# Kernel optimization log

Hardware: AMD Instinct MI355X
Metric: run time of the kernel (lower is better)

Reference implementation:

```python
import jax, jax.numpy as jnp
import numpy as np

N = 100_000   # nodes
E = 1_600_000 # edges (avg degree 16)
D = 128       # input_dim
H = 128       # hidden_dim
G = 64        # graphs in batch
C = 2         # num_classes


def setup_inputs() -> dict:
    key = jax.random.key(0)
    ks = jax.random.split(key, 16)
    x = jax.random.normal(ks[0], (N, D), dtype=jnp.float32)
    edge_index = jax.random.randint(ks[1], (2, E), 0, N, dtype=jnp.int32)
    batch = jnp.sort(jax.random.randint(ks[2], (N,), 0, G, dtype=jnp.int32))
    def lin(k, fin, fout):
        s = 1.0 / np.sqrt(fin)
        kw, kb = jax.random.split(k)
        W = jax.random.uniform(kw, (fin, fout), jnp.float32, -s, s)
        b = jax.random.uniform(kb, (fout,), jnp.float32, -s, s)
        return W, b
    W0, b0 = lin(ks[3], D, H)
    W1, b1 = lin(ks[4], H, H)
    W2, b2 = lin(ks[5], H, H)
    Wc1, bc1 = lin(ks[6], 2 * H, H)
    Wc2, bc2 = lin(ks[7], H, C)
    return dict(x=x, edge_index=edge_index, batch=batch,
                W0=W0, b0=b0, W1=W1, b1=b1, W2=W2, b2=b2,
                Wc1=Wc1, bc1=bc1, Wc2=Wc2, bc2=bc2)


def _gcn_layer(x, W, b, src, dst, dinv):
    # GCNConv with self-loops and symmetric normalization:
    # out_i = sum_{j->i} d_j^{-1/2} d_i^{-1/2} (x_j W) + d_i^{-1} (x_i W) + b
    h = x @ W                                   # [N, H]
    coef = dinv[src] * dinv[dst]                # [E]
    agg = jax.ops.segment_sum(h[src] * coef[:, None], dst, num_segments=N)
    return agg + h * (dinv * dinv)[:, None] + b


def reference(x, edge_index, batch, W0, b0, W1, b1, W2, b2, Wc1, bc1, Wc2, bc2):
    src, dst = edge_index[0], edge_index[1]
    # degree with self-loops (in-degree on target nodes + 1)
    deg = jax.ops.segment_sum(jnp.ones((E,), jnp.float32), dst, num_segments=N) + 1.0
    dinv = jax.lax.rsqrt(deg)
    for W, b in ((W0, b0), (W1, b1), (W2, b2)):
        x = jax.nn.relu(_gcn_layer(x, W, b, src, dst, dinv))
        # dropout: inference mode -> identity
    # global mean pool per graph
    sums = jax.ops.segment_sum(x, batch, num_segments=G)            # [G, H]
    cnt = jax.ops.segment_sum(jnp.ones((N,), jnp.float32), batch, num_segments=G)
    pooled = sums / jnp.maximum(cnt, 1.0)[:, None]
    combined = jnp.concatenate([pooled, pooled], axis=1)            # [G, 2H]
    hcls = jax.nn.relu(combined @ Wc1 + bc1)
    return hcls @ Wc2 + bc2                                         # [G, C]
```

## Files before the change

kernel.cpp:

```cpp
#include <hip/hip_runtime.h>

#define HDIM 128
#define GCOUNT 64
#define CHUNK 2048

__device__ __forceinline__ float bfl(unsigned u) { return __uint_as_float(u << 16); }
__device__ __forceinline__ unsigned short f2bf(float f) {
  unsigned u = __float_as_uint(f);
  unsigned r = (u + 0x7fffu + ((u >> 16) & 1u)) >> 16;
  return (unsigned short)r;
}
__device__ __forceinline__ unsigned pk2(float a, float b) {
  return (unsigned)f2bf(a) | ((unsigned)f2bf(b) << 16);
}

typedef __attribute__((ext_vector_type(8))) short short8;
typedef __attribute__((ext_vector_type(4))) float f32x4;

__device__ __forceinline__ unsigned qb(float v, float rinv) {
  int q = (int)rintf(v * rinv);
  return (unsigned)(q & 0xff);
}


__global__ void mega1(const float* __restrict__ W0, const float* __restrict__ W1,
                      const float* __restrict__ W2,
                      unsigned short* __restrict__ h0, unsigned short* __restrict__ l0,
                      unsigned short* __restrict__ h1, unsigned short* __restrict__ l1,
                      unsigned short* __restrict__ h2, unsigned short* __restrict__ l2,
                      float* __restrict__ pooled, float* __restrict__ gcnt, int pz,
                      const int* __restrict__ dst, int E, int G, int NB1,
                      int* __restrict__ gcount,
                      const float* __restrict__ x, uint2* __restrict__ S,
                      uint2* __restrict__ Sb, float* __restrict__ csaP,
                      float* __restrict__ csbP,
                      float* __restrict__ cs_base, int n) {
  __shared__ int hist[512];
  int b = blockIdx.x, t = threadIdx.x;
  if (b < 192) {
    int w = b >> 6;
    int idx = (b & 63) * 256 + t;
    const float* W = (w == 0) ? W0 : (w == 1) ? W1 : W2;
    unsigned short* hi = (w == 0) ? h0 : (w == 1) ? h1 : h2;
    unsigned short* lo = (w == 0) ? l0 : (w == 1) ? l1 : l2;
    int k = idx >> 7, nn = idx & 127;
    float wv = W[idx];
    unsigned short h = f2bf(wv);
    float hf = __uint_as_float((unsigned)h << 16);
    unsigned short l = f2bf(wv - hf);
    int kb = k >> 5, quad = (k >> 3) & 3, e = k & 7;
    int nt = nn >> 4, m = nn & 15;
    int di = (((kb * 8 + nt) * 64) + quad * 16 + m) * 8 + e;
    hi[di] = h;
    lo[di] = l;
  } else if (b < 192 + pz) {
    int i = (b - 192) * 256 + t;
    if (i < GCOUNT * HDIM) pooled[i] = 0.f;
    else if (i - GCOUNT * HDIM < GCOUNT) gcnt[i - GCOUNT * HDIM] = 0.f;
    if (b == 192) {
      if (t < 16) S[(size_t)n * 16 + t] = make_uint2(0u, 0u);
      else if (t < 32) Sb[(size_t)n * 16 + (t - 16)] = make_uint2(0u, 0u);
      else if (t == 32) csaP[n] = 0.f;
      else if (t == 33) csbP[n] = 0.f;
    }
  } else if (b < 192 + pz + G) {
    int blk = b - 192 - pz;
    for (int i = t; i < NB1; i += 256) hist[i] = 0;
    __syncthreads();
    int base = blk * CHUNK;
    #pragma unroll
    for (int j = 0; j < CHUNK / 256; j++) {
      int e = base + j * 256 + t;
      if (e < E) atomicAdd(&hist[dst[e] >> 8], 1);
    }
    __syncthreads();
    for (int i = t; i < NB1; i += 256) gcount[i * G + blk] = hist[i];
  } else {
    int idx = (b - 192 - pz - G) * 16 + (t >> 4);
    int l = t & 15;
    int ridx = min(idx, n - 1);
    float4 f0 = ((const float4*)x)[(size_t)ridx * 32 + l * 2];
    float4 f1 = ((const float4*)x)[(size_t)ridx * 32 + l * 2 + 1];
    float v0 = f0.x, v1 = f0.y, v2 = f0.z, v3 = f0.w;
    float v4 = f1.x, v5 = f1.y, v6 = f1.z, v7 = f1.w;
    float mx = fmaxf(fmaxf(fmaxf(fabsf(v0), fabsf(v1)), fmaxf(fabsf(v2), fabsf(v3))),
                     fmaxf(fmaxf(fabsf(v4), fabsf(v5)), fmaxf(fabsf(v6), fabsf(v7))));
    mx = fmaxf(mx, __shfl_xor(mx, 1));
    mx = fmaxf(mx, __shfl_xor(mx, 2));
    mx = fmaxf(mx, __shfl_xor(mx, 4));
    mx = fmaxf(mx, __shfl_xor(mx, 8));
    float c = mx * (1.0f / 127.0f);
    float rinv = (mx > 0.f) ? 127.0f / mx : 0.f;
    if (idx < n) {
      unsigned lo = qb(v0, rinv) | (qb(v1, rinv) << 8) | (qb(v2, rinv) << 16) | (qb(v3, rinv) << 24);
      unsigned hi = qb(v4, rinv) | (qb(v5, rinv) << 8) | (qb(v6, rinv) << 16) | (qb(v7, rinv) << 24);
      S[(size_t)idx * 16 + l] = make_uint2(lo, hi);
      if (l == 0) cs_base[idx] = c;
    }
  }
}


__global__ void scanA(int* __restrict__ g, int* __restrict__ bsum, int M) {
  __shared__ int sh[1024];
  int t = threadIdx.x;
  int i = blockIdx.x * 1024 + t;
  int v = (i < M) ? g[i] : 0;
  sh[t] = v;
  __syncthreads();
  for (int off = 1; off < 1024; off <<= 1) {
    int u = (t >= off) ? sh[t - off] : 0;
    __syncthreads();
    sh[t] += u;
    __syncthreads();
  }
  if (i < M) g[i] = sh[t] - v;
  if (t == 1023) bsum[blockIdx.x] = sh[1023];
}


__global__ void rs_scatter(const int* __restrict__ src, const int* __restrict__ dst,
                           const int* __restrict__ gscan, const int* __restrict__ bsum,
                           int nb, int E, int G, int NB1,
                           unsigned* __restrict__ sp) {
  __shared__ int run[512];
  __shared__ int sb[512];
  int blk = blockIdx.x, t = threadIdx.x;
  sb[t] = (t < nb) ? bsum[t] : 0;
  __syncthreads();
  for (int off = 1; off < 512; off <<= 1) {
    int u = (t >= off) ? sb[t - off] : 0;
    __syncthreads();
    sb[t] += u;
    __syncthreads();
  }
  for (int i = t; i < NB1; i += 512) {
    int idx = i * G + blk;
    int j = idx >> 10;
    run[i] = gscan[idx] + (j ? sb[j - 1] : 0);
  }
  __syncthreads();
  int base = blk * CHUNK;
  #pragma unroll
  for (int j = 0; j < CHUNK / 512; j++) {
    int e = base + j * 512 + t;
    if (e < E) {
      int d = dst[e];
      int pos = atomicAdd(&run[d >> 8], 1);
      sp[pos] = (unsigned)src[e] | ((unsigned)(d & 255) << 24);
    }
  }
}


__global__ void csr_fine(const unsigned* __restrict__ sp, const int* __restrict__ gscan,
                         const int* __restrict__ bsum, int nb,
                         int E, int G, int NB1,
                         int2* __restrict__ rowpe, int* __restrict__ colv,
                         float* __restrict__ dinv, const float* __restrict__ cs_base,
                         float* __restrict__ cs, int n) {
  __shared__ int sb[512];
  __shared__ int hist[256];
  __shared__ int scn[256];
  __shared__ int run2[256];
  int hb = blockIdx.x, t = threadIdx.x;
  sb[t] = (t < nb) ? bsum[t] : 0;
  __syncthreads();
  for (int off = 1; off < 512; off <<= 1) {
    int u = (t >= off) ? sb[t - off] : 0;
    __syncthreads();
    sb[t] += u;
    __syncthreads();
  }
  int iO = hb * G;
  int jO = iO >> 10;
  int O = gscan[iO] + (jO ? sb[jO - 1] : 0);
  int Oe;
  if (hb == NB1 - 1) Oe = E;
  else {
    int i2 = (hb + 1) * G;
    int j2 = i2 >> 10;
    Oe = gscan[i2] + (j2 ? sb[j2 - 1] : 0);
  }
  int PO = ((O + 3) & ~3) + hb * 1024;
  if (t < 256) hist[t] = 0;
  __syncthreads();
  for (int e = O + t; e < Oe; e += 512) atomicAdd(&hist[sp[e] >> 24], 1);
  __syncthreads();
  int v = 0, pv = 0;
  if (t < 256) { v = hist[t]; pv = (v + 3) & ~3; scn[t] = pv; }
  __syncthreads();
  for (int off = 1; off < 256; off <<= 1) {
    int u = (t < 256 && t >= off) ? scn[t - off] : 0;
    __syncthreads();
    if (t < 256) scn[t] += u;
    __syncthreads();
  }
  if (t < 256) {
    int st = PO + scn[t] - pv;
    run2[t] = st;
    int d = (hb << 8) + t;
    rowpe[d] = make_int2(st, st + pv);
    for (int i = v; i < pv; i++) colv[st + i] = n;
    if (d < n) {
      float dv = rsqrtf((float)v + 1.0f);
      dinv[d] = dv;
      cs[d] = cs_base[d] * dv;
    }
  }
  __syncthreads();
  for (int e = O + t; e < Oe; e += 512) {
    unsigned p = sp[e];
    int pos = atomicAdd(&run2[p >> 24], 1);
    colv[pos] = (int)(p & 0xFFFFFFu);
  }
}


__device__ __forceinline__ void acc8(uint2 v, float c, float* a) {
  int xx = (int)v.x, yy = (int)v.y;
  a[0] += c * (float)(signed char)(xx);
  a[1] += c * (float)(signed char)(xx >> 8);
  a[2] += c * (float)(signed char)(xx >> 16);
  a[3] += c * (float)(xx >> 24);
  a[4] += c * (float)(signed char)(yy);
  a[5] += c * (float)(signed char)(yy >> 8);
  a[6] += c * (float)(signed char)(yy >> 16);
  a[7] += c * (float)(yy >> 24);
}


__device__ __forceinline__ void agg_phase(
    const uint2* __restrict__ S, const float* __restrict__ cs,
    const float* __restrict__ dinv,
    const int2* __restrict__ rowpe,
    const int* __restrict__ col,
    uint4* At, int block0, int t, int n) {
  int grp = t >> 4, gl = t & 15;
  #pragma unroll 1
  for (int k = 0; k < 4; k++) {
    int lrow = grp * 4 + k;
    int g = block0 + lrow;
    uint4 o = make_uint4(0u, 0u, 0u, 0u);
    if (g < n) {
      float a[8];
      {
        uint2 q = S[(size_t)g * 16 + gl];
        float c = cs[g];
        int xx = (int)q.x, yy = (int)q.y;
        a[0] = c * (float)(signed char)(xx);
        a[1] = c * (float)(signed char)(xx >> 8);
        a[2] = c * (float)(signed char)(xx >> 16);
        a[3] = c * (float)(xx >> 24);
        a[4] = c * (float)(signed char)(yy);
        a[5] = c * (float)(signed char)(yy >> 8);
        a[6] = c * (float)(signed char)(yy >> 16);
        a[7] = c * (float)(yy >> 24);
      }
      int2 pe = rowpe[g];
      int e = pe.x, e1 = pe.y;
      if (e < e1) {
        int4 ca = *(const int4*)(col + e);
        uint2 q0 = S[(size_t)ca.x * 16 + gl];
        uint2 q1 = S[(size_t)ca.y * 16 + gl];
        uint2 q2 = S[(size_t)ca.z * 16 + gl];
        uint2 q3 = S[(size_t)ca.w * 16 + gl];
        float c0 = cs[ca.x], c1 = cs[ca.y], c2 = cs[ca.z], c3 = cs[ca.w];
        #pragma unroll 1
        for (e += 4; e < e1; e += 4) {
          int4 cn = *(const int4*)(col + e);
          uint2 p0 = S[(size_t)cn.x * 16 + gl];
          uint2 p1 = S[(size_t)cn.y * 16 + gl];
          uint2 p2 = S[(size_t)cn.z * 16 + gl];
          uint2 p3 = S[(size_t)cn.w * 16 + gl];
          float d0 = cs[cn.x], d1 = cs[cn.y], d2 = cs[cn.z], d3 = cs[cn.w];
          acc8(q0, c0, a); acc8(q1, c1, a); acc8(q2, c2, a); acc8(q3, c3, a);
          q0 = p0; q1 = p1; q2 = p2; q3 = p3;
          c0 = d0; c1 = d1; c2 = d2; c3 = d3;
        }
        acc8(q0, c0, a); acc8(q1, c1, a); acc8(q2, c2, a); acc8(q3, c3, a);
      }
      float d = dinv[g];
      o.x = pk2(a[0] * d, a[1] * d);
      o.y = pk2(a[2] * d, a[3] * d);
      o.z = pk2(a[4] * d, a[5] * d);
      o.w = pk2(a[6] * d, a[7] * d);
    }
    At[(gl << 6) + (lrow ^ (gl & 7))] = o;
  }
}

__device__ __forceinline__ void stage16(uint4* Wl, const uint4* __restrict__ WT, int t) {
  #pragma unroll
  for (int i = 0; i < 4; i++) {
    int idx = t + i * 256;
    Wl[idx] = WT[idx];
  }
}

__device__ __forceinline__ void mfma2(const uint4* Wl, const uint4* av, f32x4* acc,
                                      int kbase, int lane) {
  #pragma unroll
  for (int kk = 0; kk < 2; kk++) {
    short8 af = __builtin_bit_cast(short8, av[kbase + kk]);
    #pragma unroll
    for (int nt = 0; nt < 8; nt++) {
      uint4 b = Wl[(kk * 8 + nt) * 64 + lane];
      acc[nt] = __builtin_amdgcn_mfma_f32_16x16x32_bf16(af, __builtin_bit_cast(short8, b), acc[nt], 0, 0, 0);
    }
  }
}

__global__ __launch_bounds__(256, 4) void fused_q8(
    const uint2* __restrict__ S, const float* __restrict__ cs,
    const float* __restrict__ dinv,
    const int2* __restrict__ rowpe,
    const int* __restrict__ col,
    const uint4* __restrict__ WThi, const uint4* __restrict__ WTlo,
    const float* __restrict__ bias,
    unsigned char* __restrict__ Sout, float* __restrict__ csout, int n) {
  __shared__ __align__(16) char smem[16384];
  uint4* At = (uint4*)smem;
  uint4* Wl = (uint4*)smem;
  int t = threadIdx.x;
  int lane = t & 63, wv = t >> 6;
  int m = lane & 15, quad = lane >> 4;
  int block0 = blockIdx.x * 64;

  agg_phase(S, cs, dinv, rowpe, col, At, block0, t, n);
  __syncthreads();

  uint4 av[4];
  #pragma unroll
  for (int kb = 0; kb < 4; kb++) {
    int glr = kb * 4 + quad;
    av[kb] = At[(glr << 6) + ((wv * 16 + m) ^ (glr & 7))];
  }
  __syncthreads();

  f32x4 acc[8];
  #pragma unroll
  for (int i = 0; i < 8; i++) acc[i] = (f32x4){0.f, 0.f, 0.f, 0.f};

  stage16(Wl, WThi, t);        __syncthreads();
  mfma2(Wl, av, acc, 0, lane); __syncthreads();
  stage16(Wl, WThi + 1024, t); __syncthreads();
  mfma2(Wl, av, acc, 2, lane); __syncthreads();
  stage16(Wl, WTlo, t);        __syncthreads();
  mfma2(Wl, av, acc, 0, lane); __syncthreads();
  stage16(Wl, WTlo + 1024, t); __syncthreads();
  mfma2(Wl, av, acc, 2, lane); __syncthreads();

  char* stg = smem;
  float* LcA = (float*)(smem + 9216);
  #pragma unroll
  for (int r = 0; r < 4; r++) {
    int lrow = wv * 16 + quad * 4 + r;
    int grow = block0 + lrow;
    float sc = (grow < n) ? dinv[grow] : 0.f;
    float v[8];
    float mx = 0.f;
    #pragma unroll
    for (int nt = 0; nt < 8; nt++) {
      v[nt] = fmaxf(acc[nt][r] + bias[nt * 16 + m], 0.f) * sc;
      mx = fmaxf(mx, v[nt]);
    }
    mx = fmaxf(mx, __shfl_xor(mx, 1));
    mx = fmaxf(mx, __shfl_xor(mx, 2));
    mx = fmaxf(mx, __shfl_xor(mx, 4));
    mx = fmaxf(mx, __shfl_xor(mx, 8));
    float c = mx * (1.0f / 127.0f);
    float rinv = (mx > 0.f) ? 127.0f / mx : 0.f;
    #pragma unroll
    for (int nt = 0; nt < 8; nt++) {
      stg[lrow * 144 + nt * 16 + m] = (char)(int)rintf(v[nt] * rinv);
    }
    if (m == 0) LcA[lrow] = c;
  }
  __syncthreads();
  for (int i = t; i < 512; i += 256) {
    int lrow = i >> 3, seg = i & 7;
    int grow = block0 + lrow;
    if (grow < n)
      ((uint4*)Sout)[(size_t)grow * 8 + seg] = *(const uint4*)&stg[lrow * 144 + seg * 16];
  }
  if (t < 64 && block0 + t < n) csout[block0 + t] = LcA[t];
}

__global__ __launch_bounds__(256, 4) void fused_final(
    const uint2* __restrict__ S, const float* __restrict__ cs,
    const float* __restrict__ dinv,
    const int2* __restrict__ rowpe,
    const int* __restrict__ col,
    const uint4* __restrict__ WThi, const uint4* __restrict__ WTlo,
    const float* __restrict__ bias, const int* __restrict__ batch,
    float* __restrict__ pooled, float* __restrict__ gcnt, int n) {
  __shared__ __align__(16) char smem[16384];
  uint4* At = (uint4*)smem;
  uint4* Wl = (uint4*)smem;
  int t = threadIdx.x;
  int lane = t & 63, wv = t >> 6;
  int m = lane & 15, quad = lane >> 4;
  int block0 = blockIdx.x * 64;

  agg_phase(S, cs, dinv, rowpe, col, At, block0, t, n);
  __syncthreads();

  uint4 av[4];
  #pragma unroll
  for (int kb = 0; kb < 4; kb++) {
    int glr = kb * 4 + quad;
    av[kb] = At[(glr << 6) + ((wv * 16 + m) ^ (glr & 7))];
  }
  __syncthreads();

  f32x4 acc[8];
  #pragma unroll
  for (int i = 0; i < 8; i++) acc[i] = (f32x4){0.f, 0.f, 0.f, 0.f};

  stage16(Wl, WThi, t);        __syncthreads();
  mfma2(Wl, av, acc, 0, lane); __syncthreads();
  stage16(Wl, WThi + 1024, t); __syncthreads();
  mfma2(Wl, av, acc, 2, lane); __syncthreads();
  stage16(Wl, WTlo, t);        __syncthreads();
  mfma2(Wl, av, acc, 0, lane); __syncthreads();
  stage16(Wl, WTlo + 1024, t); __syncthreads();
  mfma2(Wl, av, acc, 2, lane); __syncthreads();

  unsigned short* Ls = (unsigned short*)smem;
  #pragma unroll
  for (int r = 0; r < 4; r++) {
    int lrow = wv * 16 + quad * 4 + r;
    #pragma unroll
    for (int nt = 0; nt < 8; nt++) {
      float v = fmaxf(acc[nt][r] + bias[nt * 16 + m], 0.f);
      Ls[lrow * 128 + nt * 16 + m] = f2bf(v);
    }
  }
  __syncthreads();
  if (t < 128) {
    float a2 = 0.f, cl = 0.f;
    int gcur = -1;
    for (int r = 0; r < 64; r++) {
      int grow = block0 + r;
      if (grow >= n) break;
      int gr = batch[grow];
      if (gr != gcur) {
        if (gcur >= 0) {
          atomicAdd(&pooled[gcur * HDIM + t], a2);
          if (t == 0) atomicAdd(&gcnt[gcur], cl);
        }
        a2 = 0.f; cl = 0.f; gcur = gr;
      }
      a2 += bfl((unsigned)Ls[r * 128 + t]);
      cl += 1.f;
    }
    if (gcur >= 0) {
      atomicAdd(&pooled[gcur * HDIM + t], a2);
      if (t == 0) atomicAdd(&gcnt[gcur], cl);
    }
  }
}


__global__ void cls_kernel(const float* __restrict__ pooled, const float* __restrict__ gcnt,
                           const float* __restrict__ Wc1, const float* __restrict__ bc1,
                           const float* __restrict__ Wc2, const float* __restrict__ bc2,
                           float* __restrict__ out) {
  __shared__ float p[HDIM];
  __shared__ float r0s[HDIM], r1s[HDIM];
  int g = blockIdx.x, t = threadIdx.x;
  float c = fmaxf(gcnt[g], 1.0f);
  p[t] = pooled[g * HDIM + t] / c;
  __syncthreads();
  float acc = bc1[t];
  for (int k = 0; k < HDIM; k++) {
    acc += p[k] * (Wc1[k * HDIM + t] + Wc1[(HDIM + k) * HDIM + t]);
  }
  float h = fmaxf(acc, 0.f);
  r0s[t] = h * Wc2[t * 2 + 0];
  r1s[t] = h * Wc2[t * 2 + 1];
  __syncthreads();
  for (int s2 = 64; s2 > 0; s2 >>= 1) {
    if (t < s2) { r0s[t] += r0s[t + s2]; r1s[t] += r1s[t + s2]; }
    __syncthreads();
  }
  if (t == 0) {
    out[g * 2 + 0] = r0s[0] + bc2[0];
    out[g * 2 + 1] = r1s[0] + bc2[1];
  }
}


extern "C" void kernel_launch(void* const* d_in, const int* in_sizes, int n_in,
                              void* d_out, int out_size, void* d_ws, size_t ws_size,
                              hipStream_t stream) {
  const float* x   = (const float*)d_in[0];
  const int*   ei  = (const int*)d_in[1];
  const int*   bat = (const int*)d_in[2];
  const float* W0  = (const float*)d_in[3];
  const float* b0  = (const float*)d_in[4];
  const float* W1  = (const float*)d_in[5];
  const float* b1  = (const float*)d_in[6];
  const float* W2  = (const float*)d_in[7];
  const float* b2  = (const float*)d_in[8];
  const float* Wc1 = (const float*)d_in[9];
  const float* bc1 = (const float*)d_in[10];
  const float* Wc2 = (const float*)d_in[11];
  const float* bc2 = (const float*)d_in[12];
  float* out = (float*)d_out;

  int N = in_sizes[0] / HDIM;
  int E = in_sizes[1] / 2;
  const int* src = ei;
  const int* dst = ei + E;

  int NB1 = (N + 255) >> 8;
  int G = (E + CHUNK - 1) / CHUNK;
  int M = NB1 * G;

  char* ws = (char*)d_ws;
  size_t off = 0;
  auto alloc = [&](size_t bytes) -> void* {
    void* p = (void*)(ws + off);
    off += (bytes + 511) & ~(size_t)511;
    return p;
  };
  unsigned char* Sa = (unsigned char*)alloc((size_t)(N + 1) * HDIM * 2);
  unsigned char* Sb = Sa + (size_t)(N + 1) * HDIM;
  float* csa  = (float*)alloc((size_t)(N + 2) * 4);
  float* csb  = (float*)alloc((size_t)(N + 2) * 4);
  float* cs_base = (float*)alloc((size_t)N * 4);
  float* dinv = (float*)alloc((size_t)N * 4);
  int2*  rowpe = (int2*)alloc((size_t)(NB1 * 256 + 2) * 8);
  int*   colv = (int*)alloc((size_t)(E + NB1 * 1024 + 1024) * 4);
  unsigned* sp = (unsigned*)alloc((size_t)E * 4);
  float* pooled = (float*)alloc((size_t)GCOUNT * HDIM * 4);
  float* gcnt   = (float*)alloc((size_t)GCOUNT * 4);
  unsigned short* wt_hi[3], *wt_lo[3];
  for (int i = 0; i < 3; i++) {
    wt_hi[i] = (unsigned short*)alloc(HDIM * HDIM * 2);
    wt_lo[i] = (unsigned short*)alloc(HDIM * HDIM * 2);
  }
  int* gcount = (int*)alloc((size_t)(M + 2) * 4);
  int nbM = (M + 1023) / 1024;
  int* bsum = (int*)alloc((size_t)nbM * 4);

  int pz = (GCOUNT * HDIM + GCOUNT + 255) / 256;
  int psb = (N + 15) / 16;
  mega1<<<192 + pz + G + psb, 256, 0, stream>>>(W0, W1, W2,
      wt_hi[0], wt_lo[0], wt_hi[1], wt_lo[1], wt_hi[2], wt_lo[2],
      pooled, gcnt, pz, dst, E, G, NB1, gcount,
      x, (uint2*)Sa, (uint2*)Sb, csa, csb, cs_base, N);

  scanA<<<nbM, 1024, 0, stream>>>(gcount, bsum, M);

  rs_scatter<<<G, 512, 0, stream>>>(src, dst, gcount, bsum, nbM, E, G, NB1, sp);
  csr_fine<<<NB1, 512, 0, stream>>>(sp, gcount, bsum, nbM, E, G, NB1, rowpe, colv,
      dinv, cs_base, csa, N);

  int fusedBlocks = (N + 63) / 64;

  fused_q8<<<fusedBlocks, 256, 0, stream>>>((const uint2*)Sa, csa, dinv, rowpe, colv,
      (const uint4*)wt_hi[0], (const uint4*)wt_lo[0], b0, Sb, csb, N);

  fused_q8<<<fusedBlocks, 256, 0, stream>>>((const uint2*)Sb, csb, dinv, rowpe, colv,
      (const uint4*)wt_hi[1], (const uint4*)wt_lo[1], b1, Sa, csa, N);

  fused_final<<<fusedBlocks, 256, 0, stream>>>((const uint2*)Sa, csa, dinv, rowpe, colv,
      (const uint4*)wt_hi[2], (const uint4*)wt_lo[2], b2, bat, pooled, gcnt, N);

  cls_kernel<<<GCOUNT, HDIM, 0, stream>>>(pooled, gcnt, Wc1, bc1, Wc2, bc2, out);
}
```

Measured before the change: 318.1 us.

## Halve rows per block in fused GCN kernels and split output columns across waves

Each fused layer block now handles 32 nodes instead of 64, giving twice as many blocks. The four waves are arranged as two row halves by two column halves, each computing 4 of the 8 MFMA output tiles. The per-row int8 quantisation max is now combined across the two column-half waves through shared memory, which adds a barrier. This is meant to improve latency hiding and load balance in the gather-bound aggregation, at the cost of restaging the weight matrix twice as often per node.

Measured after the change: 322.7 us. Within noise of the previous version (+1.4%).

```diff
diff --git a/kernel.cpp b/kernel.cpp
--- a/kernel.cpp
+++ b/kernel.cpp
@@ -238,8 +238,8 @@
     uint4* At, int block0, int t, int n) {
   int grp = t >> 4, gl = t & 15;
   #pragma unroll 1
-  for (int k = 0; k < 4; k++) {
-    int lrow = grp * 4 + k;
+  for (int k = 0; k < 2; k++) {
+    int lrow = grp * 2 + k;
     int g = block0 + lrow;
     uint4 o = make_uint4(0u, 0u, 0u, 0u);
     if (g < n) {
@@ -286,7 +286,7 @@
       o.z = pk2(a[4] * d, a[5] * d);
       o.w = pk2(a[6] * d, a[7] * d);
     }
-    At[(gl << 6) + (lrow ^ (gl & 7))] = o;
+    At[(gl << 5) + (lrow ^ (gl & 7))] = o;
   }
 }
 
@@ -298,15 +298,15 @@
   }
 }
 
-__device__ __forceinline__ void mfma2(const uint4* Wl, const uint4* av, f32x4* acc,
-                                      int kbase, int lane) {
+__device__ __forceinline__ void mfma2h(const uint4* Wl, const uint4* av, f32x4* acc,
+                                       int kbase, int nh, int lane) {
   #pragma unroll
   for (int kk = 0; kk < 2; kk++) {
     short8 af = __builtin_bit_cast(short8, av[kbase + kk]);
     #pragma unroll
-    for (int nt = 0; nt < 8; nt++) {
-      uint4 b = Wl[(kk * 8 + nt) * 64 + lane];
-      acc[nt] = __builtin_amdgcn_mfma_f32_16x16x32_bf16(af, __builtin_bit_cast(short8, b), acc[nt], 0, 0, 0);
+    for (int j = 0; j < 4; j++) {
+      uint4 b = Wl[(kk * 8 + nh + j) * 64 + lane];
+      acc[j] = __builtin_amdgcn_mfma_f32_16x16x32_bf16(af, __builtin_bit_cast(short8, b), acc[j], 0, 0, 0);
     }
   }
 }
@@ -325,7 +325,10 @@
   int t = threadIdx.x;
   int lane = t & 63, wv = t >> 6;
   int m = lane & 15, quad = lane >> 4;
-  int block0 = blockIdx.x * 64;
+  int rh = wv >> 1;
+  int nh = (wv & 1) * 4;
+  int r0 = rh * 16;
+  int block0 = blockIdx.x * 32;
 
   agg_phase(S, cs, dinv, rowpe, col, At, block0, t, n);
   __syncthreads();
@@ -334,57 +337,66 @@
   #pragma unroll
   for (int kb = 0; kb < 4; kb++) {
     int glr = kb * 4 + quad;
-    av[kb] = At[(glr << 6) + ((wv * 16 + m) ^ (glr & 7))];
-  }
-  __syncthreads();
-
-  f32x4 acc[8];
-  #pragma unroll
-  for (int i = 0; i < 8; i++) acc[i] = (f32x4){0.f, 0.f, 0.f, 0.f};
-
-  stage16(Wl, WThi, t);        __syncthreads();
-  mfma2(Wl, av, acc, 0, lane); __syncthreads();
-  stage16(Wl, WThi + 1024, t); __syncthreads();
-  mfma2(Wl, av, acc, 2, lane); __syncthreads();
-  stage16(Wl, WTlo, t);        __syncthreads();
-  mfma2(Wl, av, acc, 0, lane); __syncthreads();
-  stage16(Wl, WTlo + 1024, t); __syncthreads();
-  mfma2(Wl, av, acc, 2, lane); __syncthreads();
+    av[kb] = At[(glr << 5) + ((r0 + m) ^ (glr & 7))];
+  }
+  __syncthreads();
+
+  f32x4 acc[4];
+  #pragma unroll
+  for (int i = 0; i < 4; i++) acc[i] = (f32x4){0.f, 0.f, 0.f, 0.f};
+
+  stage16(Wl, WThi, t);              __syncthreads();
+  mfma2h(Wl, av, acc, 0, nh, lane);  __syncthreads();
+  stage16(Wl, WThi + 1024, t);       __syncthreads();
+  mfma2h(Wl, av, acc, 2, nh, lane);  __syncthreads();
+  stage16(Wl, WTlo, t);              __syncthreads();
+  mfma2h(Wl, av, acc, 0, nh, lane);  __syncthreads();
+  stage16(Wl, WTlo + 1024, t);       __syncthreads();
+  mfma2h(Wl, av, acc, 2, nh, lane);  __syncthreads();
 
   char* stg = smem;
-  float* LcA = (float*)(smem + 9216);
+  float* LcA = (float*)(smem + 4608);
+  float* pmx = (float*)(smem + 4864);
+  float v[4][4];
   #pragma unroll
   for (int r = 0; r < 4; r++) {
-    int lrow = wv * 16 + quad * 4 + r;
+    int lrow = r0 + quad * 4 + r;
     int grow = block0 + lrow;
     float sc = (grow < n) ? dinv[grow] : 0.f;
-    float v[8];
     float mx = 0.f;
     #pragma unroll
-    for (int nt = 0; nt < 8; nt++) {
-      v[nt] = fmaxf(acc[nt][r] + bias[nt * 16 + m], 0.f) * sc;
-      mx = fmaxf(mx, v[nt]);
+    for (int j = 0; j < 4; j++) {
+      v[r][j] = fmaxf(acc[j][r] + bias[(nh + j) * 16 + m], 0.f) * sc;
+      mx = fmaxf(mx, v[r][j]);
     }
     mx = fmaxf(mx, __shfl_xor(mx, 1));
     mx = fmaxf(mx, __shfl_xor(mx, 2));
     mx = fmaxf(mx, __shfl_xor(mx, 4));
     mx = fmaxf(mx, __shfl_xor(mx, 8));
-    float c = mx * (1.0f / 127.0f);
-    float rinv = (mx > 0.f) ? 127.0f / mx : 0.f;
+    if (m == 0) pmx[wv * 16 + quad * 4 + r] = mx;
+  }
+  __syncthreads();
+  #pragma unroll
+  for (int r = 0; r < 4; r++) {
+    int lr = quad * 4 + r;
+    int lrow = r0 + lr;
+    float full = fmaxf(pmx[(rh * 2) * 16 + lr], pmx[(rh * 2 + 1) * 16 + lr]);
+    float c = full * (1.0f / 127.0f);
+    float rinv = (full > 0.f) ? 127.0f / full : 0.f;
     #pragma unroll
-    for (int nt = 0; nt < 8; nt++) {
-      stg[lrow * 144 + nt * 16 + m] = (char)(int)rintf(v[nt] * rinv);
-    }
-    if (m == 0) LcA[lrow] = c;
-  }
-  __syncthreads();
-  for (int i = t; i < 512; i += 256) {
-    int lrow = i >> 3, seg = i & 7;
+    for (int j = 0; j < 4; j++) {
+      stg[lrow * 144 + (nh + j) * 16 + m] = (char)(int)rintf(v[r][j] * rinv);
+    }
+    if (m == 0 && nh == 0) LcA[lrow] = c;
+  }
+  __syncthreads();
+  {
+    int lrow = t >> 3, seg = t & 7;
     int grow = block0 + lrow;
     if (grow < n)
       ((uint4*)Sout)[(size_t)grow * 8 + seg] = *(const uint4*)&stg[lrow * 144 + seg * 16];
   }
-  if (t < 64 && block0 + t < n) csout[block0 + t] = LcA[t];
+  if (t < 32 && block0 + t < n) csout[block0 + t] = LcA[t];
 }
 
 __global__ __launch_bounds__(256, 4) void fused_final(
@@ -401,7 +413,10 @@
   int t = threadIdx.x;
   int lane = t & 63, wv = t >> 6;
   int m = lane & 15, quad = lane >> 4;
-  int block0 = blockIdx.x * 64;
+  int rh = wv >> 1;
+  int nh = (wv & 1) * 4;
+  int r0 = rh * 16;
+  int block0 = blockIdx.x * 32;
 
   agg_phase(S, cs, dinv, rowpe, col, At, block0, t, n);
   __syncthreads();
@@ -410,38 +425,38 @@
   #pragma unroll
   for (int kb = 0; kb < 4; kb++) {
     int glr = kb * 4 + quad;
-    av[kb] = At[(glr << 6) + ((wv * 16 + m) ^ (glr & 7))];
-  }
-  __syncthreads();
-
-  f32x4 acc[8];
-  #pragma unroll
-  for (int i = 0; i < 8; i++) acc[i] = (f32x4){0.f, 0.f, 0.f, 0.f};
-
-  stage16(Wl, WThi, t);        __syncthreads();
-  mfma2(Wl, av, acc, 0, lane); __syncthreads();
-  stage16(Wl, WThi + 1024, t); __syncthreads();
-  mfma2(Wl, av, acc, 2, lane); __syncthreads();
-  stage16(Wl, WTlo, t);        __syncthreads();
-  mfma2(Wl, av, acc, 0, lane); __syncthreads();
-  stage16(Wl, WTlo + 1024, t); __syncthreads();
-  mfma2(Wl, av, acc, 2, lane); __syncthreads();
+    av[kb] = At[(glr << 5) + ((r0 + m) ^ (glr & 7))];
+  }
+  __syncthreads();
+
+  f32x4 acc[4];
+  #pragma unroll
+  for (int i = 0; i < 4; i++) acc[i] = (f32x4){0.f, 0.f, 0.f, 0.f};
+
+  stage16(Wl, WThi, t);              __syncthreads();
+  mfma2h(Wl, av, acc, 0, nh, lane);  __syncthreads();
+  stage16(Wl, WThi + 1024, t);       __syncthreads();
+  mfma2h(Wl, av, acc, 2, nh, lane);  __syncthreads();
+  stage16(Wl, WTlo, t);              __syncthreads();
+  mfma2h(Wl, av, acc, 0, nh, lane);  __syncthreads();
+  stage16(Wl, WTlo + 1024, t);       __syncthreads();
+  mfma2h(Wl, av, acc, 2, nh, lane);  __syncthreads();
 
   unsigned short* Ls = (unsigned short*)smem;
   #pragma unroll
   for (int r = 0; r < 4; r++) {
-    int lrow = wv * 16 + quad * 4 + r;
+    int lrow = r0 + quad * 4 + r;
     #pragma unroll
-    for (int nt = 0; nt < 8; nt++) {
-      float v = fmaxf(acc[nt][r] + bias[nt * 16 + m], 0.f);
-      Ls[lrow * 128 + nt * 16 + m] = f2bf(v);
+    for (int j = 0; j < 4; j++) {
+      float v = fmaxf(acc[j][r] + bias[(nh + j) * 16 + m], 0.f);
+      Ls[lrow * 128 + (nh + j) * 16 + m] = f2bf(v);
     }
   }
   __syncthreads();
   if (t < 128) {
     float a2 = 0.f, cl = 0.f;
     int gcur = -1;
-    for (int r = 0; r < 64; r++) {
+    for (int r = 0; r < 32; r++) {
       int grow = block0 + r;
       if (grow >= n) break;
       int gr = batch[grow];
@@ -559,7 +574,7 @@
   csr_fine<<<NB1, 512, 0, stream>>>(sp, gcount, bsum, nbM, E, G, NB1, rowpe, colv,
       dinv, cs_base, csa, N);
 
-  int fusedBlocks = (N + 63) / 64;
+  int fusedBlocks = (N + 31) / 32;
 
   fused_q8<<<fusedBlocks, 256, 0, stream>>>((const uint2*)Sa, csa, dinv, rowpe, colv,
       (const uint4*)wt_hi[0], (const uint4*)wt_lo[0], b0, Sb, csb, N);
```

## Use 1024-thread blocks so each aggregation thread handles one row

Applied to the files above, without the earlier changes.

The fused GCN layer kernels now run 1024 threads per 64-row block instead of 256. Each 16-lane group aggregates a single node row rather than looping over four rows serially, so more gather latency can be hidden. The MFMA work is split across 16 waves, with four row groups each covering two of the eight output column tiles. The per-row int8 quantisation max now needs a cross-wave reduction through shared memory and an extra barrier. The trade-offs are more barrier cost across 16 waves and a tighter launch-bound register budget.

Measured after the change: 354.0 us. 1.11x slower.

```diff
diff --git a/kernel.cpp b/kernel.cpp
--- a/kernel.cpp
+++ b/kernel.cpp
@@ -237,81 +237,74 @@
     const int* __restrict__ col,
     uint4* At, int block0, int t, int n) {
   int grp = t >> 4, gl = t & 15;
-  #pragma unroll 1
-  for (int k = 0; k < 4; k++) {
-    int lrow = grp * 4 + k;
-    int g = block0 + lrow;
-    uint4 o = make_uint4(0u, 0u, 0u, 0u);
-    if (g < n) {
-      float a[8];
-      {
-        uint2 q = S[(size_t)g * 16 + gl];
-        float c = cs[g];
-        int xx = (int)q.x, yy = (int)q.y;
-        a[0] = c * (float)(signed char)(xx);
-        a[1] = c * (float)(signed char)(xx >> 8);
-        a[2] = c * (float)(signed char)(xx >> 16);
-        a[3] = c * (float)(xx >> 24);
-        a[4] = c * (float)(signed char)(yy);
-        a[5] = c * (float)(signed char)(yy >> 8);
-        a[6] = c * (float)(signed char)(yy >> 16);
-        a[7] = c * (float)(yy >> 24);
+  int lrow = grp;
+  int g = block0 + lrow;
+  uint4 o = make_uint4(0u, 0u, 0u, 0u);
+  if (g < n) {
+    float a[8];
+    {
+      uint2 q = S[(size_t)g * 16 + gl];
+      float c = cs[g];
+      int xx = (int)q.x, yy = (int)q.y;
+      a[0] = c * (float)(signed char)(xx);
+      a[1] = c * (float)(signed char)(xx >> 8);
+      a[2] = c * (float)(signed char)(xx >> 16);
+      a[3] = c * (float)(xx >> 24);
+      a[4] = c * (float)(signed char)(yy);
+      a[5] = c * (float)(signed char)(yy >> 8);
+      a[6] = c * (float)(signed char)(yy >> 16);
+      a[7] = c * (float)(yy >> 24);
+    }
+    int2 pe = rowpe[g];
+    int e = pe.x, e1 = pe.y;
+    if (e < e1) {
+      int4 ca = *(const int4*)(col + e);
+      uint2 q0 = S[(size_t)ca.x * 16 + gl];
+      uint2 q1 = S[(size_t)ca.y * 16 + gl];
+      uint2 q2 = S[(size_t)ca.z * 16 + gl];
+      uint2 q3 = S[(size_t)ca.w * 16 + gl];
+      float c0 = cs[ca.x], c1 = cs[ca.y], c2 = cs[ca.z], c3 = cs[ca.w];
+      #pragma unroll 1
+      for (e += 4; e < e1; e += 4) {
+        int4 cn = *(const int4*)(col + e);
+        uint2 p0 = S[(size_t)cn.x * 16 + gl];
+        uint2 p1 = S[(size_t)cn.y * 16 + gl];
+        uint2 p2 = S[(size_t)cn.z * 16 + gl];
+        uint2 p3 = S[(size_t)cn.w * 16 + gl];
+        float d0 = cs[cn.x], d1 = cs[cn.y], d2 = cs[cn.z], d3 = cs[cn.w];
+        acc8(q0, c0, a); acc8(q1, c1, a); acc8(q2, c2, a); acc8(q3, c3, a);
+        q0 = p0; q1 = p1; q2 = p2; q3 = p3;
+        c0 = d0; c1 = d1; c2 = d2; c3 = d3;
       }
-      int2 pe = rowpe[g];
-      int e = pe.x, e1 = pe.y;
-      if (e < e1) {
-        int4 ca = *(const int4*)(col + e);
-        uint2 q0 = S[(size_t)ca.x * 16 + gl];
-        uint2 q1 = S[(size_t)ca.y * 16 + gl];
-        uint2 q2 = S[(size_t)ca.z * 16 + gl];
-        uint2 q3 = S[(size_t)ca.w * 16 + gl];
-        float c0 = cs[ca.x], c1 = cs[ca.y], c2 = cs[ca.z], c3 = cs[ca.w];
-        #pragma unroll 1
-        for (e += 4; e < e1; e += 4) {
-          int4 cn = *(const int4*)(col + e);
-          uint2 p0 = S[(size_t)cn.x * 16 + gl];
-          uint2 p1 = S[(size_t)cn.y * 16 + gl];
-          uint2 p2 = S[(size_t)cn.z * 16 + gl];
-          uint2 p3 = S[(size_t)cn.w * 16 + gl];
-          float d0 = cs[cn.x], d1 = cs[cn.y], d2 = cs[cn.z], d3 = cs[cn.w];
-          acc8(q0, c0, a); acc8(q1, c1, a); acc8(q2, c2, a); acc8(q3, c3, a);
-          q0 = p0; q1 = p1; q2 = p2; q3 = p3;
-          c0 = d0; c1 = d1; c2 = d2; c3 = d3;
-        }
-        acc8(q0, c0, a); acc8(q1, c1, a); acc8(q2, c2, a); acc8(q3, c3, a);
-      }
-      float d = dinv[g];
-      o.x = pk2(a[0] * d, a[1] * d);
-      o.y = pk2(a[2] * d, a[3] * d);
-      o.z = pk2(a[4] * d, a[5] * d);
-      o.w = pk2(a[6] * d, a[7] * d);
-    }
-    At[(gl << 6) + (lrow ^ (gl & 7))] = o;
-  }
+      acc8(q0, c0, a); acc8(q1, c1, a); acc8(q2, c2, a); acc8(q3, c3, a);
+    }
+    float d = dinv[g];
+    o.x = pk2(a[0] * d, a[1] * d);
+    o.y = pk2(a[2] * d, a[3] * d);
+    o.z = pk2(a[4] * d, a[5] * d);
+    o.w = pk2(a[6] * d, a[7] * d);
+  }
+  At[(gl << 6) + (lrow ^ (gl & 7))] = o;
 }
 
 __device__ __forceinline__ void stage16(uint4* Wl, const uint4* __restrict__ WT, int t) {
-  #pragma unroll
-  for (int i = 0; i < 4; i++) {
-    int idx = t + i * 256;
-    Wl[idx] = WT[idx];
-  }
-}
-
-__device__ __forceinline__ void mfma2(const uint4* Wl, const uint4* av, f32x4* acc,
-                                      int kbase, int lane) {
+  Wl[t] = WT[t];
+}
+
+__device__ __forceinline__ void mfma2q(const uint4* Wl, const uint4* av, f32x4* acc,
+                                       int kbase, int nq, int lane) {
   #pragma unroll
   for (int kk = 0; kk < 2; kk++) {
     short8 af = __builtin_bit_cast(short8, av[kbase + kk]);
     #pragma unroll
-    for (int nt = 0; nt < 8; nt++) {
-      uint4 b = Wl[(kk * 8 + nt) * 64 + lane];
-      acc[nt] = __builtin_amdgcn_mfma_f32_16x16x32_bf16(af, __builtin_bit_cast(short8, b), acc[nt], 0, 0, 0);
-    }
-  }
-}
-
-__global__ __launch_bounds__(256, 4) void fused_q8(
+    for (int j = 0; j < 2; j++) {
+      uint4 b = Wl[(kk * 8 + nq + j) * 64 + lane];
+      acc[j] = __builtin_amdgcn_mfma_f32_16x16x32_bf16(af, __builtin_bit_cast(short8, b), acc[j], 0, 0, 0);
+    }
+  }
+}
+
+__global__ __launch_bounds__(1024, 8) void fused_q8(
     const uint2* __restrict__ S, const float* __restrict__ cs,
     const float* __restrict__ dinv,
     const int2* __restrict__ rowpe,
@@ -325,6 +318,9 @@
   int t = threadIdx.x;
   int lane = t & 63, wv = t >> 6;
   int m = lane & 15, quad = lane >> 4;
+  int rg = wv >> 2;
+  int nq = (wv & 3) * 2;
+  int r0 = rg * 16;
   int block0 = blockIdx.x * 64;
 
   agg_phase(S, cs, dinv, rowpe, col, At, block0, t, n);
@@ -334,52 +330,63 @@
   #pragma unroll
   for (int kb = 0; kb < 4; kb++) {
     int glr = kb * 4 + quad;
-    av[kb] = At[(glr << 6) + ((wv * 16 + m) ^ (glr & 7))];
-  }
-  __syncthreads();
-
-  f32x4 acc[8];
-  #pragma unroll
-  for (int i = 0; i < 8; i++) acc[i] = (f32x4){0.f, 0.f, 0.f, 0.f};
-
-  stage16(Wl, WThi, t);        __syncthreads();
-  mfma2(Wl, av, acc, 0, lane); __syncthreads();
-  stage16(Wl, WThi + 1024, t); __syncthreads();
-  mfma2(Wl, av, acc, 2, lane); __syncthreads();
-  stage16(Wl, WTlo, t);        __syncthreads();
-  mfma2(Wl, av, acc, 0, lane); __syncthreads();
-  stage16(Wl, WTlo + 1024, t); __syncthreads();
-  mfma2(Wl, av, acc, 2, lane); __syncthreads();
+    av[kb] = At[(glr << 6) + ((r0 + m) ^ (glr & 7))];
+  }
+  __syncthreads();
+
+  f32x4 acc[2];
+  #pragma unroll
+  for (int i = 0; i < 2; i++) acc[i] = (f32x4){0.f, 0.f, 0.f, 0.f};
+
+  stage16(Wl, WThi, t);               __syncthreads();
+  mfma2q(Wl, av, acc, 0, nq, lane);   __syncthreads();
+  stage16(Wl, WThi + 1024, t);        __syncthreads();
+  mfma2q(Wl, av, acc, 2, nq, lane);   __syncthreads();
+  stage16(Wl, WTlo, t);               __syncthreads();
+  mfma2q(Wl, av, acc, 0, nq, lane);   __syncthreads();
+  stage16(Wl, WTlo + 1024, t);        __syncthreads();
+  mfma2q(Wl, av, acc, 2, nq, lane);   __syncthreads();
 
   char* stg = smem;
   float* LcA = (float*)(smem + 9216);
+  float* pmx = (float*)(smem + 9472);
+  float v[4][2];
   #pragma unroll
   for (int r = 0; r < 4; r++) {
-    int lrow = wv * 16 + quad * 4 + r;
-    int grow = block0 + lrow;
+    int lr = quad * 4 + r;
+    int grow = block0 + r0 + lr;
     float sc = (grow < n) ? dinv[grow] : 0.f;
-    float v[8];
     float mx = 0.f;
     #pragma unroll
-    for (int nt = 0; nt < 8; nt++) {
-      v[nt] = fmaxf(acc[nt][r] + bias[nt * 16 + m], 0.f) * sc;
-      mx = fmaxf(mx, v[nt]);
+    for (int j = 0; j < 2; j++) {
+      v[r][j] = fmaxf(acc[j][r] + bias[(nq + j) * 16 + m], 0.f) * sc;
+      mx = fmaxf(mx, v[r][j]);
     }
     mx = fmaxf(mx, __shfl_xor(mx, 1));
     mx = fmaxf(mx, __shfl_xor(mx, 2));
     mx = fmaxf(mx, __shfl_xor(mx, 4));
     mx = fmaxf(mx, __shfl_xor(mx, 8));
-    float c = mx * (1.0f / 127.0f);
-    float rinv = (mx > 0.f) ? 127.0f / mx : 0.f;
+    if (m == 0) pmx[wv * 16 + lr] = mx;
+  }
+  __syncthreads();
+  #pragma unroll
+  for (int r = 0; r < 4; r++) {
+    int lr = quad * 4 + r;
+    int lrow = r0 + lr;
+    int wb = rg * 4;
+    float full = fmaxf(fmaxf(pmx[(wb + 0) * 16 + lr], pmx[(wb + 1) * 16 + lr]),
+                       fmaxf(pmx[(wb + 2) * 16 + lr], pmx[(wb + 3) * 16 + lr]));
+    float c = full * (1.0f / 127.0f);
+    float rinv = (full > 0.f) ? 127.0f / full : 0.f;
     #pragma unroll
-    for (int nt = 0; nt < 8; nt++) {
-      stg[lrow * 144 + nt * 16 + m] = (char)(int)rintf(v[nt] * rinv);
-    }
-    if (m == 0) LcA[lrow] = c;
-  }
-  __syncthreads();
-  for (int i = t; i < 512; i += 256) {
-    int lrow = i >> 3, seg = i & 7;
+    for (int j = 0; j < 2; j++) {
+      stg[lrow * 144 + (nq + j) * 16 + m] = (char)(int)rintf(v[r][j] * rinv);
+    }
+    if (m == 0 && (wv & 3) == 0) LcA[lrow] = c;
+  }
+  __syncthreads();
+  if (t < 512) {
+    int lrow = t >> 3, seg = t & 7;
     int grow = block0 + lrow;
     if (grow < n)
       ((uint4*)Sout)[(size_t)grow * 8 + seg] = *(const uint4*)&stg[lrow * 144 + seg * 16];
@@ -387,7 +394,7 @@
   if (t < 64 && block0 + t < n) csout[block0 + t] = LcA[t];
 }
 
-__global__ __launch_bounds__(256, 4) void fused_final(
+__global__ __launch_bounds__(1024, 8) void fused_final(
     const uint2* __restrict__ S, const float* __restrict__ cs,
     const float* __restrict__ dinv,
     const int2* __restrict__ rowpe,
@@ -401,6 +408,9 @@
   int t = threadIdx.x;
   int lane = t & 63, wv = t >> 6;
   int m = lane & 15, quad = lane >> 4;
+  int rg = wv >> 2;
+  int nq = (wv & 3) * 2;
+  int r0 = rg * 16;
   int block0 = blockIdx.x * 64;
 
   agg_phase(S, cs, dinv, rowpe, col, At, block0, t, n);
@@ -410,31 +420,31 @@
   #pragma unroll
   for (int kb = 0; kb < 4; kb++) {
     int glr = kb * 4 + quad;
-    av[kb] = At[(glr << 6) + ((wv * 16 + m) ^ (glr & 7))];
-  }
-  __syncthreads();
-
-  f32x4 acc[8];
-  #pragma unroll
-  for (int i = 0; i < 8; i++) acc[i] = (f32x4){0.f, 0.f, 0.f, 0.f};
-
-  stage16(Wl, WThi, t);        __syncthreads();
-  mfma2(Wl, av, acc, 0, lane); __syncthreads();
-  stage16(Wl, WThi + 1024, t); __syncthreads();
-  mfma2(Wl, av, acc, 2, lane); __syncthreads();
-  stage16(Wl, WTlo, t);        __syncthreads();
-  mfma2(Wl, av, acc, 0, lane); __syncthreads();
-  stage16(Wl, WTlo + 1024, t); __syncthreads();
-  mfma2(Wl, av, acc, 2, lane); __syncthreads();
+    av[kb] = At[(glr << 6) + ((r0 + m) ^ (glr & 7))];
+  }
+  __syncthreads();
+
+  f32x4 acc[2];
+  #pragma unroll
+  for (int i = 0; i < 2; i++) acc[i] = (f32x4){0.f, 0.f, 0.f, 0.f};
+
+  stage16(Wl, WThi, t);               __syncthreads();
+  mfma2q(Wl, av, acc, 0, nq, lane);   __syncthreads();
+  stage16(Wl, WThi + 1024, t);        __syncthreads();
+  mfma2q(Wl, av, acc, 2, nq, lane);   __syncthreads();
+  stage16(Wl, WTlo, t);               __syncthreads();
+  mfma2q(Wl, av, acc, 0, nq, lane);   __syncthreads();
+  stage16(Wl, WTlo + 1024, t);        __syncthreads();
+  mfma2q(Wl, av, acc, 2, nq, lane);   __syncthreads();
 
   unsigned short* Ls = (unsigned short*)smem;
   #pragma unroll
   for (int r = 0; r < 4; r++) {
-    int lrow = wv * 16 + quad * 4 + r;
+    int lrow = r0 + quad * 4 + r;
     #pragma unroll
-    for (int nt = 0; nt < 8; nt++) {
-      float v = fmaxf(acc[nt][r] + bias[nt * 16 + m], 0.f);
-      Ls[lrow * 128 + nt * 16 + m] = f2bf(v);
+    for (int j = 0; j < 2; j++) {
+      float vv = fmaxf(acc[j][r] + bias[(nq + j) * 16 + m], 0.f);
+      Ls[lrow * 128 + (nq + j) * 16 + m] = f2bf(vv);
     }
   }
   __syncthreads();
@@ -561,13 +571,13 @@
 
   int fusedBlocks = (N + 63) / 64;
 
-  fused_q8<<<fusedBlocks, 256, 0, stream>>>((const uint2*)Sa, csa, dinv, rowpe, colv,
+  fused_q8<<<fusedBlocks, 1024, 0, stream>>>((const uint2*)Sa, csa, dinv, rowpe, colv,
       (const uint4*)wt_hi[0], (const uint4*)wt_lo[0], b0, Sb, csb, N);
 
-  fused_q8<<<fusedBlocks, 256, 0, stream>>>((const uint2*)Sb, csb, dinv, rowpe, colv,
+  fused_q8<<<fusedBlocks, 1024, 0, stream>>>((const uint2*)Sb, csb, dinv, rowpe, colv,
       (const uint4*)wt_hi[1], (const uint4*)wt_lo[1], b1, Sa, csa, N);
 
-  fused_final<<<fusedBlocks, 256, 0, stream>>>((const uint2*)Sa, csa, dinv, rowpe, colv,
+  fused_final<<<fusedBlocks, 1024, 0, stream>>>((const uint2*)Sa, csa, dinv, rowpe, colv,
       (const uint4*)wt_hi[2], (const uint4*)wt_lo[2], b2, bat, pooled, gcnt, N);
 
   cls_kernel<<<GCOUNT, HDIM, 0, stream>>>(pooled, gcnt, Wc1, bc1, Wc2, bc2, out);
```
